# Kernel optimization log

Hardware: AMD Instinct MI355X
Metric: run time of the kernel (lower is better)

## Reference

```python
import jax, jax.numpy as jnp
import numpy as np

N_NODES = 100000
N_EDGES = 1700000  # 1.6M random edges + 100k self-loops (dgl.add_self_loop)
HID = 128
N_GRAPHS = 64
N_CLASSES = 10
T_STEPS = 5


def setup_inputs() -> dict:
    key = jax.random.key(0)
    ks = jax.random.split(key, 12)
    m = jax.random.normal(ks[0], (N_NODES,), dtype=jnp.float32)
    n_rand = N_EDGES - N_NODES
    src_r = jax.random.randint(ks[1], (n_rand,), 0, N_NODES)
    dst_r = jax.random.randint(ks[2], (n_rand,), 0, N_NODES)
    loops = jnp.arange(N_NODES)
    src = jnp.concatenate([src_r, loops])
    dst = jnp.concatenate([dst_r, loops])
    graph_ids = jnp.sort(jax.random.randint(ks[3], (N_NODES,), 0, N_GRAPHS))
    s = 0.05
    W_e = jax.random.normal(ks[4], (HID, HID), dtype=jnp.float32) * s
    b_e = jnp.zeros((HID,), dtype=jnp.float32)
    W_ih = jax.random.normal(ks[5], (3 * HID, HID), dtype=jnp.float32) * s
    b_ih = jnp.zeros((3 * HID,), dtype=jnp.float32)
    W_hh = jax.random.normal(ks[6], (3 * HID, HID), dtype=jnp.float32) * s
    b_hh = jnp.zeros((3 * HID,), dtype=jnp.float32)
    W_cls = jax.random.normal(ks[7], (N_CLASSES, HID), dtype=jnp.float32) * s
    b_cls = jnp.zeros((N_CLASSES,), dtype=jnp.float32)
    return {"m": m, "W_e": W_e, "b_e": b_e, "W_ih": W_ih, "b_ih": b_ih,
            "W_hh": W_hh, "b_hh": b_hh, "W_cls": W_cls, "b_cls": b_cls,
            "src": src, "dst": dst, "graph_ids": graph_ids, "n_graphs": N_GRAPHS}


def _gated_graph_forward(m, W_e, b_e, W_ih, b_ih, W_hh, b_hh, W_cls, b_cls,
                         src, dst, graph_ids, n_graphs):
    n_nodes = m.shape[0]
    hid = W_e.shape[0]
    # h = ndata['m'].view(-1,1), zero-padded to out_feats (DGL GatedGraphConv)
    h = jnp.zeros((n_nodes, hid), dtype=m.dtype).at[:, 0].set(m)
    for _ in range(T_STEPS):
        # single edge type: a[v] = sum_{(u,v) in E} W_e h[u] + b_e
        msg = (h @ W_e.T + b_e)[src]                       # [E, H]
        a = jax.ops.segment_sum(msg, dst, num_segments=n_nodes)
        # torch.nn.GRUCell(a, h); gate order: r, z, n
        gi = a @ W_ih.T + b_ih
        gh = h @ W_hh.T + b_hh
        i_r, i_z, i_n = jnp.split(gi, 3, axis=-1)
        h_r, h_z, h_n = jnp.split(gh, 3, axis=-1)
        r = jax.nn.sigmoid(i_r + h_r)
        z = jax.nn.sigmoid(i_z + h_z)
        n = jnp.tanh(i_n + r * h_n)
        h = (1.0 - z) * n + z * h
    h = jax.nn.relu(h)
    # dgl.mean_nodes: per-graph mean over nodes
    sums = jax.ops.segment_sum(h, graph_ids, num_segments=n_graphs)
    cnt = jax.ops.segment_sum(jnp.ones((n_nodes,), h.dtype), graph_ids,
                              num_segments=n_graphs)
    hg = sums / jnp.maximum(cnt, 1.0)[:, None]             # [G, H]
    return hg @ W_cls.T + b_cls                            # [G, C]


def reference(m, W_e, b_e, W_ih, b_ih, W_hh, b_hh, W_cls, b_cls,
              src, dst, graph_ids, n_graphs):
    return _gated_graph_forward(m, W_e, b_e, W_ih, b_ih, W_hh, b_hh,
                                W_cls, b_cls, src, dst, graph_ids, n_graphs)
```

## Files before the change

### kernel.cpp

```cpp
#include <hip/hip_runtime.h>

#define HID 128
#define G3  384
#define TSTEPS 5
#define BSHIFT 9
#define BNODES (1 << BSHIFT)
#define MAXBUK 256
#define PART_EPB 8192
#define DBUK 64

typedef unsigned int  uint;
typedef unsigned short ushort;

typedef float  f32x4  __attribute__((ext_vector_type(4)));
typedef __bf16 bf16x8 __attribute__((ext_vector_type(8)));

union B8u { uint4 u; bf16x8 b; ushort s[8]; };

static __device__ inline ushort f2bf(float f) {
  uint u = __float_as_uint(f);
  uint r = u + 0x7fffu + ((u >> 16) & 1u);
  return (ushort)(r >> 16);
}
static __device__ inline float bf2f(ushort s) {
  return __uint_as_float(((uint)s) << 16);
}

__global__ __launch_bounds__(128) void k_weights(
    const float* __restrict__ W_e, const float* __restrict__ b_e,
    const float* __restrict__ W_ih, const float* __restrict__ W_hh,
    ushort* __restrict__ Wcomb, ushort* __restrict__ Whh16, float* __restrict__ bvec,
    ushort* __restrict__ Wc0, ushort* __restrict__ Wh0)
{
  int j = blockIdx.x, t = threadIdx.x;
  if (j < G3) {
    __shared__ float row[HID];
    row[t] = W_ih[j * HID + t];
    __syncthreads();
    float acc = 0.f;
    for (int k = 0; k < HID; ++k) acc = fmaf(row[k], W_e[k * HID + t], acc);
    Wcomb[j * HID + t] = f2bf(acc);
    if (t == 0) {
      Wc0[j] = f2bf(acc);
      float b = 0.f;
      for (int k = 0; k < HID; ++k) b += row[k] * b_e[k];
      bvec[j] = b;
    }
  } else {
    int j2 = j - G3;
    Whh16[j2 * HID + t] = f2bf(W_hh[j2 * HID + t]);
    if (t == 0) Wh0[j2] = f2bf(W_hh[j2 * HID]);
  }
}

__global__ __launch_bounds__(256) void k_bh(const int* __restrict__ dst,
                                            int* __restrict__ bhist, int E) {
  __shared__ int lh[MAXBUK];
  int t = threadIdx.x;
  if (t < MAXBUK) lh[t] = 0;
  __syncthreads();
  for (int e = blockIdx.x * 256 + t; e < E; e += gridDim.x * 256)
    atomicAdd(&lh[dst[e] >> BSHIFT], 1);
  __syncthreads();
  if (t < MAXBUK && lh[t]) atomicAdd(&bhist[t], lh[t]);
}

__global__ __launch_bounds__(256) void k_bsc(const int* __restrict__ bhist,
                                             int* __restrict__ bbase,
                                             int* __restrict__ gcur,
                                             int* __restrict__ rowptr, int E, int N) {
  __shared__ int ls[MAXBUK];
  int t = threadIdx.x;
  ls[t] = bhist[t];
  __syncthreads();
  if (t == 0) {
    int run = 0;
    for (int i = 0; i < MAXBUK; ++i) {
      bbase[i] = run; gcur[i] = run; run += ls[i];
    }
    bbase[MAXBUK] = run;
    rowptr[N] = E;
  }
}

__global__ __launch_bounds__(256) void k_part(
    const int* __restrict__ src, const int* __restrict__ dst,
    int* __restrict__ gcur, uint* __restrict__ ebuf, int E) {
  __shared__ int lh[MAXBUK], lbase[MAXBUK], lcur[MAXBUK];
  int t = threadIdx.x;
  int base = blockIdx.x * PART_EPB;
  if (t < MAXBUK) lh[t] = 0;
  __syncthreads();
#pragma unroll 4
  for (int j = 0; j < PART_EPB / 256; ++j) {
    int e = base + j * 256 + t;
    if (e < E) atomicAdd(&lh[dst[e] >> BSHIFT], 1);
  }
  __syncthreads();
  if (t < MAXBUK) {
    lbase[t] = lh[t] ? atomicAdd(&gcur[t], lh[t]) : 0;
    lcur[t] = 0;
  }
  __syncthreads();
#pragma unroll 4
  for (int j = 0; j < PART_EPB / 256; ++j) {
    int e = base + j * 256 + t;
    if (e < E) {
      int d = dst[e];
      int b = d >> BSHIFT;
      int p = atomicAdd(&lcur[b], 1);
      ebuf[lbase[b] + p] = (uint)src[e] | ((uint)(d & (BNODES - 1)) << 20);
    }
  }
}

__global__ __launch_bounds__(256) void k_fill2(
    const uint* __restrict__ ebuf, const int* __restrict__ bbase,
    int* __restrict__ csrc, int* __restrict__ rowptr, int* __restrict__ deg, int N) {
  __shared__ int hcnt[BNODES];
  __shared__ int wls[4];
  int t = threadIdx.x;
  int b = blockIdx.x;
  int ebeg = bbase[b], eend = bbase[b + 1];
  for (int i = t; i < BNODES; i += 256) hcnt[i] = 0;
  __syncthreads();
  for (int e = ebeg + t; e < eend; e += 256)
    atomicAdd(&hcnt[ebuf[e] >> 20], 1);
  __syncthreads();
  const int PER = BNODES / 256;
  int lane = t & 63, wv = t >> 6;
  int x[PER]; int s = 0;
#pragma unroll
  for (int i = 0; i < PER; ++i) { x[i] = hcnt[PER * t + i]; s += x[i]; }
  int incl = s;
#pragma unroll
  for (int off = 1; off < 64; off <<= 1) {
    int u = __shfl_up(incl, off, 64);
    if (lane >= off) incl += u;
  }
  if (lane == 63) wls[wv] = incl;
  __syncthreads();
  int wbase = 0;
  for (int i = 0; i < wv; ++i) wbase += wls[i];
  int run = wbase + incl - s;
#pragma unroll
  for (int i = 0; i < PER; ++i) {
    int node = (b << BSHIFT) + PER * t + i;
    hcnt[PER * t + i] = run;
    if (node < N) { rowptr[node] = ebeg + run; deg[node] = x[i]; }
    run += x[i];
  }
  __syncthreads();
  for (int e = ebeg + t; e < eend; e += 256) {
    uint v = ebuf[e];
    int p = atomicAdd(&hcnt[v >> 20], 1);
    csrc[ebeg + p] = (int)(v & 0xFFFFFu);
  }
}

__global__ __launch_bounds__(256) void k_dhist(const int* __restrict__ deg,
                                               int* __restrict__ dhist, int N) {
  __shared__ int lh[DBUK];
  int t = threadIdx.x;
  if (t < DBUK) lh[t] = 0;
  __syncthreads();
  for (int v = blockIdx.x * 256 + t; v < N; v += gridDim.x * 256)
    atomicAdd(&lh[min(deg[v], DBUK - 1)], 1);
  __syncthreads();
  if (t < DBUK && lh[t]) atomicAdd(&dhist[t], lh[t]);
}

__global__ __launch_bounds__(64) void k_dscan(const int* __restrict__ dhist,
                                              int* __restrict__ dcur) {
  if (threadIdx.x == 0) {
    int run = 0;
    for (int i = 0; i < DBUK; ++i) { dcur[i] = run; run += dhist[i]; }
  }
}

__global__ __launch_bounds__(256) void k_dscatter(
    const int* __restrict__ deg, const int* __restrict__ rowptr,
    int* __restrict__ dcur, int* __restrict__ orig2,
    int* __restrict__ beg2, int* __restrict__ deg2s, int N) {
  __shared__ int lh[DBUK], lbase[DBUK], lcur[DBUK];
  int t = threadIdx.x;
  int v = blockIdx.x * 256 + t;
  if (t < DBUK) lh[t] = 0;
  __syncthreads();
  int d = 0, b = 0;
  bool valid = v < N;
  if (valid) {
    d = deg[v];
    b = min(d, DBUK - 1);
    atomicAdd(&lh[b], 1);
  }
  __syncthreads();
  if (t < DBUK) {
    lbase[t] = lh[t] ? atomicAdd(&dcur[t], lh[t]) : 0;
    lcur[t] = 0;
  }
  __syncthreads();
  if (valid) {
    int p = atomicAdd(&lcur[b], 1);
    int k = lbase[b] + p;
    orig2[k] = v;
    beg2[k] = rowptr[v];
    deg2s[k] = d;
  }
}

__global__ void k_minit(const float* __restrict__ m, ushort* __restrict__ m16, int N) {
  int v = blockIdx.x * 256 + threadIdx.x;
  if (v < N) m16[v] = f2bf(m[v]);
}

__global__ __launch_bounds__(256) void k_gather0(
    const int* __restrict__ rowptr, const int* __restrict__ csrc,
    const ushort* __restrict__ m16, ushort* __restrict__ hsum0, int N)
{
  int v = blockIdx.x * 256 + threadIdx.x;
  if (v >= N) return;
  int beg = rowptr[v], end = rowptr[v + 1];
  float a0 = 0.f, a1 = 0.f, a2 = 0.f, a3 = 0.f;
  int e = beg;
  for (; e + 16 <= end; e += 16) {
    a0 += (bf2f(m16[csrc[e + 0]]) + bf2f(m16[csrc[e + 4]])) +
          (bf2f(m16[csrc[e + 8]]) + bf2f(m16[csrc[e + 12]]));
    a1 += (bf2f(m16[csrc[e + 1]]) + bf2f(m16[csrc[e + 5]])) +
          (bf2f(m16[csrc[e + 9]]) + bf2f(m16[csrc[e + 13]]));
    a2 += (bf2f(m16[csrc[e + 2]]) + bf2f(m16[csrc[e + 6]])) +
          (bf2f(m16[csrc[e + 10]]) + bf2f(m16[csrc[e + 14]]));
    a3 += (bf2f(m16[csrc[e + 3]]) + bf2f(m16[csrc[e + 7]])) +
          (bf2f(m16[csrc[e + 11]]) + bf2f(m16[csrc[e + 15]]));
  }
  for (; e < end; e += 4) {
    if (e + 0 < end) a0 += bf2f(m16[csrc[e + 0]]);
    if (e + 1 < end) a1 += bf2f(m16[csrc[e + 1]]);
    if (e + 2 < end) a2 += bf2f(m16[csrc[e + 2]]);
    if (e + 3 < end) a3 += bf2f(m16[csrc[e + 3]]);
  }
  hsum0[v] = f2bf((a0 + a1) + (a2 + a3));
}

__global__ __launch_bounds__(256) void k_gru0(
    const ushort* __restrict__ hsum0, const ushort* __restrict__ m16,
    const int* __restrict__ deg,
    const ushort* __restrict__ Wc0, const ushort* __restrict__ Wh0,
    const float* __restrict__ bvec, const float* __restrict__ b_ih,
    const float* __restrict__ b_hh, ushort* __restrict__ hbn, int N)
{
  int idx = blockIdx.x * 256 + threadIdx.x;
  if (idx >= N * HID) return;
  int n = idx >> 7, d = idx & (HID - 1);
  float s0 = bf2f(hsum0[n]);
  float h0 = bf2f(m16[n]);
  float degf = (float)deg[n];
  float acc0 = s0 * bf2f(Wc0[d]);
  float acc1 = s0 * bf2f(Wc0[d + 128]);
  float acc2 = s0 * bf2f(Wc0[d + 256]);
  float acc3 = h0 * bf2f(Wh0[d]);
  float acc4 = h0 * bf2f(Wh0[d + 128]);
  float acc5 = h0 * bf2f(Wh0[d + 256]);
  float hold = (d == 0) ? h0 : 0.f;
  float ir = acc0 + degf * bvec[d] + b_ih[d];
  float iz = acc1 + degf * bvec[d + 128] + b_ih[d + 128];
  float in_ = acc2 + degf * bvec[d + 256] + b_ih[d + 256];
  float hr = acc3 + b_hh[d];
  float hz = acc4 + b_hh[d + 128];
  float hn = acc5 + b_hh[d + 256];
  float r = __builtin_amdgcn_rcpf(1.f + __expf(-(ir + hr)));
  float z = __builtin_amdgcn_rcpf(1.f + __expf(-(iz + hz)));
  float x2 = in_ + r * hn;
  float e2 = __expf(2.f * x2);
  float nv = 1.f - 2.f * __builtin_amdgcn_rcpf(e2 + 1.f);
  float hv = (1.f - z) * nv + z * hold;
  hbn[idx] = f2bf(hv);
}

static __device__ __forceinline__ void accum_range(
    const ushort* __restrict__ hb, const int* __restrict__ csrc,
    int beg, int end, int g, int i, float acc[8])
{
  int e = beg;
  for (; e + 16 <= end; e += 16) {
    int s0 = csrc[e + g];
    int s1 = csrc[e + 4 + g];
    int s2 = csrc[e + 8 + g];
    int s3 = csrc[e + 12 + g];
    B8u w0; w0.u = *(const uint4*)(hb + (size_t)s0 * HID + i * 8);
    B8u w1; w1.u = *(const uint4*)(hb + (size_t)s1 * HID + i * 8);
    B8u w2; w2.u = *(const uint4*)(hb + (size_t)s2 * HID + i * 8);
    B8u w3; w3.u = *(const uint4*)(hb + (size_t)s3 * HID + i * 8);
#pragma unroll
    for (int j = 0; j < 8; ++j)
      acc[j] += (bf2f(w0.s[j]) + bf2f(w1.s[j])) + (bf2f(w2.s[j]) + bf2f(w3.s[j]));
  }
  int rem = end - e;
  if (rem > 0) {
    int t0 = (g < rem)      ? csrc[e + g]      : -1;
    int t1 = (4 + g < rem)  ? csrc[e + 4 + g]  : -1;
    int t2 = (8 + g < rem)  ? csrc[e + 8 + g]  : -1;
    int t3 = (12 + g < rem) ? csrc[e + 12 + g] : -1;
    B8u r0, r1, r2, r3;
    if (t0 >= 0) r0.u = *(const uint4*)(hb + (size_t)t0 * HID + i * 8);
    if (t1 >= 0) r1.u = *(const uint4*)(hb + (size_t)t1 * HID + i * 8);
    if (t2 >= 0) r2.u = *(const uint4*)(hb + (size_t)t2 * HID + i * 8);
    if (t3 >= 0) r3.u = *(const uint4*)(hb + (size_t)t3 * HID + i * 8);
    if (t0 >= 0) {
#pragma unroll
      for (int j = 0; j < 8; ++j) acc[j] += bf2f(r0.s[j]);
    }
    if (t1 >= 0) {
#pragma unroll
      for (int j = 0; j < 8; ++j) acc[j] += bf2f(r1.s[j]);
    }
    if (t2 >= 0) {
#pragma unroll
      for (int j = 0; j < 8; ++j) acc[j] += bf2f(r2.s[j]);
    }
    if (t3 >= 0) {
#pragma unroll
      for (int j = 0; j < 8; ++j) acc[j] += bf2f(r3.s[j]);
    }
  }
}

static __device__ __forceinline__ void gather_strip_sorted(
    const int* __restrict__ beg2, const int* __restrict__ deg2s,
    const int* __restrict__ orig2, const int* __restrict__ csrc,
    const ushort* __restrict__ hb,
    int strip, int w, int lane, int N,
    ushort dstS[16][128], ushort dstH[16][128], int* dstDeg, int* dstOrig)
{
  int k = strip * 16 + w;
  if (k >= N) return;
  int g = lane >> 4;
  int i = lane & 15;
  int orig = orig2[k];
  int beg = beg2[k];
  int cnt = deg2s[k];
  if (g == 1)
    *(uint4*)(&dstH[w][(i ^ (w & 7)) * 8]) =
        *(const uint4*)(hb + (size_t)orig * HID + i * 8);
  if (lane == 0) dstOrig[w] = orig;
  if (lane == 32) dstDeg[w] = cnt;
  float acc[8] = {0.f, 0.f, 0.f, 0.f, 0.f, 0.f, 0.f, 0.f};
  accum_range(hb, csrc, beg, beg + cnt, g, i, acc);
#pragma unroll
  for (int j = 0; j < 8; ++j) {
    acc[j] += __shfl_xor(acc[j], 16, 64);
    acc[j] += __shfl_xor(acc[j], 32, 64);
  }
  if (g == 0) {
    uint4 ov;
    ov.x = ((uint)f2bf(acc[1]) << 16) | (uint)f2bf(acc[0]);
    ov.y = ((uint)f2bf(acc[3]) << 16) | (uint)f2bf(acc[2]);
    ov.z = ((uint)f2bf(acc[5]) << 16) | (uint)f2bf(acc[4]);
    ov.w = ((uint)f2bf(acc[7]) << 16) | (uint)f2bf(acc[6]);
    *(uint4*)(&dstS[w][(i ^ (w & 7)) * 8]) = ov;
  }
}

__global__ __launch_bounds__(1024, 4) void k_fused(
    const int* __restrict__ beg2, const int* __restrict__ deg2s,
    const int* __restrict__ orig2, const int* __restrict__ csrc,
    const ushort* __restrict__ hbc, ushort* __restrict__ hbn,
    const ushort* __restrict__ Wcomb, const ushort* __restrict__ Whh16,
    const float* __restrict__ bvec, const float* __restrict__ b_ih,
    const float* __restrict__ b_hh, int N)
{
  __shared__ float S[6][16][132];
  __shared__ ushort AT[3][2][16][128];
  __shared__ int degT[3][16];
  __shared__ int origT[3][16];
  const int tid = threadIdx.x;
  const int w = tid >> 6;
  const int lane = tid & 63;
  const int quad = lane >> 4, l16 = lane & 15;
  const int gm = w >> 3;
  const int gw = w & 7;
  const int d0 = gw * 16;

  const ushort* Wmat = gm ? Whh16 : Wcomb;
  B8u bfr[3][4];
#pragma unroll
  for (int g = 0; g < 3; ++g)
#pragma unroll
    for (int kc = 0; kc < 4; ++kc) {
      int j = (d0 + g * 128 + l16) * HID + kc * 32 + quad * 8;
      bfr[g][kc].u = *(const uint4*)(Wmat + j);
    }

  const int ecol = tid & 127, erow0 = tid >> 7;
  const float bir = b_ih[ecol], biz = b_ih[ecol + 128], bin_ = b_ih[ecol + 256];
  const float bhr = b_hh[ecol], bhz = b_hh[ecol + 128], bhn = b_hh[ecol + 256];
  const float vr = bvec[ecol], vz = bvec[ecol + 128], vn = bvec[ecol + 256];

  const int nstrip = N >> 4;
  const int G = (int)gridDim.x;
  int s = blockIdx.x;
  if (s >= nstrip) return;

  gather_strip_sorted(beg2, deg2s, orig2, csrc, hbc, s, w, lane, N,
                      AT[0][0], AT[0][1], degT[0], origT[0]);
  asm volatile("s_waitcnt lgkmcnt(0)" ::: "memory");
  __builtin_amdgcn_sched_barrier(0);
  __builtin_amdgcn_s_barrier();

  int cur = 0;
  while (true) {
    int ns = s + G;
    bool more = ns < nstrip;
    int nxt = (cur == 2) ? 0 : cur + 1;
    if (more)
      gather_strip_sorted(beg2, deg2s, orig2, csrc, hbc, ns, w, lane, N,
                          AT[nxt][0], AT[nxt][1], degT[nxt], origT[nxt]);
    B8u af[4];
#pragma unroll
    for (int kc = 0; kc < 4; ++kc)
      af[kc].u = *(const uint4*)(&AT[cur][gm][l16][(((quad + 4 * kc) ^ (l16 & 7)) * 8)]);
    f32x4 acc[3] = {};
#pragma unroll
    for (int kc = 0; kc < 4; ++kc)
#pragma unroll
      for (int g = 0; g < 3; ++g)
        acc[g] = __builtin_amdgcn_mfma_f32_16x16x32_bf16(af[kc].b, bfr[g][kc].b, acc[g], 0, 0, 0);
    __builtin_amdgcn_s_barrier();
#pragma unroll
    for (int g = 0; g < 3; ++g)
#pragma unroll
      for (int rg = 0; rg < 4; ++rg)
        S[gm * 3 + g][quad * 4 + rg][d0 + l16] = acc[g][rg];
    asm volatile("s_waitcnt lgkmcnt(0)" ::: "memory");
    __builtin_amdgcn_sched_barrier(0);
    __builtin_amdgcn_s_barrier();
    int n0 = s << 4;
#pragma unroll
    for (int k = 0; k < 2; ++k) {
      int row = erow0 + 8 * k;
      float dgf = (float)degT[cur][row];
      int og = origT[cur][row];
      int sc = (((ecol >> 3) ^ (row & 7)) * 8) + (ecol & 7);
      float hold = bf2f(AT[cur][1][row][sc]);
      float ir  = S[0][row][ecol] + dgf * vr + bir;
      float iz  = S[1][row][ecol] + dgf * vz + biz;
      float in_ = S[2][row][ecol] + dgf * vn + bin_;
      float hr  = S[3][row][ecol] + bhr;
      float hz  = S[4][row][ecol] + bhz;
      float hn  = S[5][row][ecol] + bhn;
      float r = __builtin_amdgcn_rcpf(1.f + __expf(-(ir + hr)));
      float z = __builtin_amdgcn_rcpf(1.f + __expf(-(iz + hz)));
      float x2 = in_ + r * hn;
      float e2 = __expf(2.f * x2);
      float nv = 1.f - 2.f * __builtin_amdgcn_rcpf(e2 + 1.f);
      float hv = (1.f - z) * nv + z * hold;
      if (n0 + row < N)
        hbn[(size_t)og * HID + ecol] = f2bf(hv);
    }
    if (!more) break;
    s = ns; cur = nxt;
  }
}

__global__ __launch_bounds__(64) void k_bounds(const int* __restrict__ gid,
                                               int* __restrict__ cnt, int N, int G) {
  int g = threadIdx.x;
  if (g >= G) return;
  int lo = 0, hi = N;
  while (lo < hi) { int mid = (lo + hi) >> 1; if (gid[mid] < g) lo = mid + 1; else hi = mid; }
  int lb0 = lo;
  lo = 0; hi = N;
  int g1 = g + 1;
  while (lo < hi) { int mid = (lo + hi) >> 1; if (gid[mid] < g1) lo = mid + 1; else hi = mid; }
  cnt[g] = lo - lb0;
}

#define POOL_CHUNK 96
__global__ __launch_bounds__(128) void k_pool(const ushort* __restrict__ hb,
                                              const int* __restrict__ gid,
                                              float* __restrict__ hg, int N) {
  int d = threadIdx.x;
  int start = blockIdx.x * POOL_CHUNK;
  if (start >= N) return;
  int end = min(start + POOL_CHUNK, N);
  float acc = 0.f;
  int g = gid[start];
  for (int n = start; n < end; ++n) {
    int gn = gid[n];
    if (gn != g) { unsafeAtomicAdd(&hg[g * HID + d], acc); acc = 0.f; g = gn; }
    acc += fmaxf(bf2f(hb[(size_t)n * HID + d]), 0.f);
  }
  unsafeAtomicAdd(&hg[g * HID + d], acc);
}

__global__ __launch_bounds__(640) void k_cls(const float* __restrict__ hg,
                                             const int* __restrict__ cnt,
                                             const float* __restrict__ Wc,
                                             const float* __restrict__ bc,
                                             float* __restrict__ out, int G) {
  int t = threadIdx.x;
  if (t >= G * 10) return;
  int g = t / 10, c = t % 10;
  float inv = 1.f / fmaxf((float)cnt[g], 1.f);
  float acc = 0.f;
  for (int d = 0; d < HID; ++d) acc = fmaf(hg[g * HID + d], Wc[c * HID + d], acc);
  out[t] = acc * inv + bc[c];
}

extern "C" void kernel_launch(void* const* d_in, const int* in_sizes, int n_in,
                              void* d_out, int out_size, void* d_ws, size_t ws_size,
                              hipStream_t stream) {
  const int N = in_sizes[0];
  const int E = in_sizes[9];
  const float* m    = (const float*)d_in[0];
  const float* W_e  = (const float*)d_in[1];
  const float* b_e  = (const float*)d_in[2];
  const float* W_ih = (const float*)d_in[3];
  const float* b_ih = (const float*)d_in[4];
  const float* W_hh = (const float*)d_in[5];
  const float* b_hh = (const float*)d_in[6];
  const float* W_cls = (const float*)d_in[7];
  const float* b_cls = (const float*)d_in[8];
  const int* src = (const int*)d_in[9];
  const int* dst = (const int*)d_in[10];
  const int* gid = (const int*)d_in[11];
  const int G = out_size / 10;
  float* out = (float*)d_out;

  size_t off = 0;
  auto alloc = [&](size_t b) {
    char* p = (char*)d_ws + off;
    off += (b + 255) & ~(size_t)255;
    return (void*)p;
  };
  ushort* hb0    = (ushort*)alloc((size_t)N * HID * 2);
  ushort* hb1    = (ushort*)alloc((size_t)N * HID * 2);
  int*    deg    = (int*)   alloc((size_t)N * 4);
  int*    rowptr = (int*)   alloc((size_t)(N + 1) * 4);
  int*    csrc   = (int*)   alloc((size_t)E * 4);
  uint*   ebuf   = (uint*)  alloc((size_t)E * 4);
  int*    bhist  = (int*)   alloc((size_t)MAXBUK * 4);
  int*    bbase  = (int*)   alloc((size_t)(MAXBUK + 1) * 4);
  int*    gcur   = (int*)   alloc((size_t)MAXBUK * 4);
  ushort* Wcomb  = (ushort*)alloc((size_t)G3 * HID * 2);
  ushort* Whh16  = (ushort*)alloc((size_t)G3 * HID * 2);
  float*  bvec   = (float*) alloc((size_t)G3 * 4);
  float*  hg     = (float*) alloc((size_t)G * HID * 4);
  int*    cnt    = (int*)   alloc((size_t)G * 4);
  ushort* m16    = (ushort*)alloc((size_t)N * 2);
  ushort* hsum0  = (ushort*)alloc((size_t)N * 2);
  ushort* Wc0    = (ushort*)alloc((size_t)G3 * 2);
  ushort* Wh0    = (ushort*)alloc((size_t)G3 * 2);
  int*    dhist  = (int*)   alloc((size_t)DBUK * 4);
  int*    dcur   = (int*)   alloc((size_t)DBUK * 4);
  int*    orig2  = (int*)   alloc((size_t)N * 4);
  int*    beg2   = (int*)   alloc((size_t)N * 4);
  int*    deg2s  = (int*)   alloc((size_t)N * 4);
  if (off > ws_size) return;

  const int NBUK = (N + BNODES - 1) >> BSHIFT;

  k_weights<<<2 * G3, HID, 0, stream>>>(W_e, b_e, W_ih, W_hh, Wcomb, Whh16, bvec, Wc0, Wh0);
  k_minit<<<(N + 255) / 256, 256, 0, stream>>>(m, m16, N);
  hipMemsetAsync(bhist, 0, (size_t)MAXBUK * 4, stream);
  k_bh<<<256, 256, 0, stream>>>(dst, bhist, E);
  k_bsc<<<1, MAXBUK, 0, stream>>>(bhist, bbase, gcur, rowptr, E, N);
  k_part<<<(E + PART_EPB - 1) / PART_EPB, 256, 0, stream>>>(src, dst, gcur, ebuf, E);
  k_fill2<<<NBUK, 256, 0, stream>>>(ebuf, bbase, csrc, rowptr, deg, N);

  hipMemsetAsync(dhist, 0, (size_t)DBUK * 4, stream);
  k_dhist<<<64, 256, 0, stream>>>(deg, dhist, N);
  k_dscan<<<1, 64, 0, stream>>>(dhist, dcur);
  k_dscatter<<<(N + 255) / 256, 256, 0, stream>>>(deg, rowptr, dcur, orig2, beg2, deg2s, N);

  k_gather0<<<(N + 255) / 256, 256, 0, stream>>>(rowptr, csrc, m16, hsum0, N);
  k_gru0<<<(N * HID + 255) / 256, 256, 0, stream>>>(hsum0, m16, deg, Wc0, Wh0,
                                                    bvec, b_ih, b_hh, hb1, N);

  ushort* hbc = hb1;
  ushort* hbn = hb0;
  const int nstrip = N >> 4;
  const int fuse_blocks = nstrip < 256 ? nstrip : 256;
  for (int s = 1; s < TSTEPS; ++s) {
    k_fused<<<fuse_blocks, 1024, 0, stream>>>(beg2, deg2s, orig2, csrc, hbc, hbn,
                                              Wcomb, Whh16, bvec, b_ih, b_hh, N);
    ushort* t = hbc; hbc = hbn; hbn = t;
  }

  hipMemsetAsync(hg, 0, (size_t)G * HID * 4, stream);
  k_bounds<<<1, 64, 0, stream>>>(gid, cnt, N, G);
  k_pool<<<(N + POOL_CHUNK - 1) / POOL_CHUNK, HID, 0, stream>>>(hbc, gid, hg, N);
  k_cls<<<1, 640, 0, stream>>>(hg, cnt, W_cls, b_cls, out, G);
}
```

Before: 752.9 us.

## Double-buffer GRU staging LDS and add fast path for low-degree gathers

The shared staging array S is double-buffered by loop parity, which lets the barrier before the MFMA result store be dropped so successive strips can overlap. Gathers for nodes with degree up to 31 get a specialized unrolled path that issues all neighbor index and row loads up front, raising memory-level parallelism over the generic accumulate loop. The cost is doubled LDS use for S, which may lower occupancy, plus more registers and code in the gather routine.

```diff
diff --git a/kernel.cpp b/kernel.cpp
--- a/kernel.cpp
+++ b/kernel.cpp
@@ -345,7 +345,55 @@
   if (lane == 0) dstOrig[w] = orig;
   if (lane == 32) dstDeg[w] = cnt;
   float acc[8] = {0.f, 0.f, 0.f, 0.f, 0.f, 0.f, 0.f, 0.f};
-  accum_range(hb, csrc, beg, beg + cnt, g, i, acc);
+  if (cnt <= 31) {
+    bool hm = cnt >= 16;
+    int m0 = 0, m1 = 0, m2 = 0, m3 = 0;
+    if (hm) {
+      m0 = csrc[beg + g];
+      m1 = csrc[beg + 4 + g];
+      m2 = csrc[beg + 8 + g];
+      m3 = csrc[beg + 12 + g];
+    }
+    int tb = hm ? beg + 16 : beg;
+    int rem = hm ? cnt - 16 : cnt;
+    int t0 = (g < rem)      ? csrc[tb + g]      : -1;
+    int t1 = (4 + g < rem)  ? csrc[tb + 4 + g]  : -1;
+    int t2 = (8 + g < rem)  ? csrc[tb + 8 + g]  : -1;
+    int t3 = (12 + g < rem) ? csrc[tb + 12 + g] : -1;
+    if (hm) {
+      B8u w0, w1, w2, w3;
+      w0.u = *(const uint4*)(hb + (size_t)m0 * HID + i * 8);
+      w1.u = *(const uint4*)(hb + (size_t)m1 * HID + i * 8);
+      w2.u = *(const uint4*)(hb + (size_t)m2 * HID + i * 8);
+      w3.u = *(const uint4*)(hb + (size_t)m3 * HID + i * 8);
+#pragma unroll
+      for (int j = 0; j < 8; ++j)
+        acc[j] += (bf2f(w0.s[j]) + bf2f(w1.s[j])) + (bf2f(w2.s[j]) + bf2f(w3.s[j]));
+    }
+    B8u r0, r1, r2, r3;
+    if (t0 >= 0) r0.u = *(const uint4*)(hb + (size_t)t0 * HID + i * 8);
+    if (t1 >= 0) r1.u = *(const uint4*)(hb + (size_t)t1 * HID + i * 8);
+    if (t2 >= 0) r2.u = *(const uint4*)(hb + (size_t)t2 * HID + i * 8);
+    if (t3 >= 0) r3.u = *(const uint4*)(hb + (size_t)t3 * HID + i * 8);
+    if (t0 >= 0) {
+#pragma unroll
+      for (int j = 0; j < 8; ++j) acc[j] += bf2f(r0.s[j]);
+    }
+    if (t1 >= 0) {
+#pragma unroll
+      for (int j = 0; j < 8; ++j) acc[j] += bf2f(r1.s[j]);
+    }
+    if (t2 >= 0) {
+#pragma unroll
+      for (int j = 0; j < 8; ++j) acc[j] += bf2f(r2.s[j]);
+    }
+    if (t3 >= 0) {
+#pragma unroll
+      for (int j = 0; j < 8; ++j) acc[j] += bf2f(r3.s[j]);
+    }
+  } else {
+    accum_range(hb, csrc, beg, beg + cnt, g, i, acc);
+  }
 #pragma unroll
   for (int j = 0; j < 8; ++j) {
     acc[j] += __shfl_xor(acc[j], 16, 64);
@@ -369,7 +417,7 @@
     const float* __restrict__ bvec, const float* __restrict__ b_ih,
     const float* __restrict__ b_hh, int N)
 {
-  __shared__ float S[6][16][132];
+  __shared__ float S[2][6][16][132];
   __shared__ ushort AT[3][2][16][128];
   __shared__ int degT[3][16];
   __shared__ int origT[3][16];
@@ -407,7 +455,7 @@
   __builtin_amdgcn_sched_barrier(0);
   __builtin_amdgcn_s_barrier();
 
-  int cur = 0;
+  int cur = 0, par = 0;
   while (true) {
     int ns = s + G;
     bool more = ns < nstrip;
@@ -425,12 +473,11 @@
 #pragma unroll
       for (int g = 0; g < 3; ++g)
         acc[g] = __builtin_amdgcn_mfma_f32_16x16x32_bf16(af[kc].b, bfr[g][kc].b, acc[g], 0, 0, 0);
-    __builtin_amdgcn_s_barrier();
 #pragma unroll
     for (int g = 0; g < 3; ++g)
 #pragma unroll
       for (int rg = 0; rg < 4; ++rg)
-        S[gm * 3 + g][quad * 4 + rg][d0 + l16] = acc[g][rg];
+        S[par][gm * 3 + g][quad * 4 + rg][d0 + l16] = acc[g][rg];
     asm volatile("s_waitcnt lgkmcnt(0)" ::: "memory");
     __builtin_amdgcn_sched_barrier(0);
     __builtin_amdgcn_s_barrier();
@@ -442,12 +489,12 @@
       int og = origT[cur][row];
       int sc = (((ecol >> 3) ^ (row & 7)) * 8) + (ecol & 7);
       float hold = bf2f(AT[cur][1][row][sc]);
-      float ir  = S[0][row][ecol] + dgf * vr + bir;
-      float iz  = S[1][row][ecol] + dgf * vz + biz;
-      float in_ = S[2][row][ecol] + dgf * vn + bin_;
-      float hr  = S[3][row][ecol] + bhr;
-      float hz  = S[4][row][ecol] + bhz;
-      float hn  = S[5][row][ecol] + bhn;
+      float ir  = S[par][0][row][ecol] + dgf * vr + bir;
+      float iz  = S[par][1][row][ecol] + dgf * vz + biz;
+      float in_ = S[par][2][row][ecol] + dgf * vn + bin_;
+      float hr  = S[par][3][row][ecol] + bhr;
+      float hz  = S[par][4][row][ecol] + bhz;
+      float hn  = S[par][5][row][ecol] + bhn;
       float r = __builtin_amdgcn_rcpf(1.f + __expf(-(ir + hr)));
       float z = __builtin_amdgcn_rcpf(1.f + __expf(-(iz + hz)));
       float x2 = in_ + r * hn;
@@ -458,7 +505,7 @@
         hbn[(size_t)og * HID + ecol] = f2bf(hv);
     }
     if (!more) break;
-    s = ns; cur = nxt;
+    s = ns; cur = nxt; par ^= 1;
   }
 }
 
```

After: 778.6 us. 1.03x slower.

## Issue neighbor-row gathers as async global-to-LDS loads overlapped with MFMA

Applied to the files above, without the earlier changes.

Replaces the call to the next-strip gather with an inline version that issues up to 20 neighbor-row loads per wave directly into a new LDS staging buffer via global_load_lds. These loads are in flight while the current strip's MFMAs and the S stores run. The remaining few neighbors are loaded into registers, and high-degree nodes fall back to the existing accumulate routine. This aims to hide gather latency behind compute, at the cost of about 80KB of extra LDS, which may reduce occupancy under the 1024-thread launch bound.

```diff
diff --git a/kernel.cpp b/kernel.cpp
--- a/kernel.cpp
+++ b/kernel.cpp
@@ -24,6 +24,12 @@
 }
 static __device__ inline float bf2f(ushort s) {
   return __uint_as_float(((uint)s) << 16);
+}
+
+static __device__ __forceinline__ void gload_lds16(const void* g, void* l) {
+  __builtin_amdgcn_global_load_lds(
+      (const __attribute__((address_space(1))) uint*)g,
+      (__attribute__((address_space(3))) uint*)l, 16, 0, 0);
 }
 
 __global__ __launch_bounds__(128) void k_weights(
@@ -373,6 +379,7 @@
   __shared__ ushort AT[3][2][16][128];
   __shared__ int degT[3][16];
   __shared__ int origT[3][16];
+  __shared__ ushort STG[16][5][512];
   const int tid = threadIdx.x;
   const int w = tid >> 6;
   const int lane = tid & 63;
@@ -412,25 +419,105 @@
     int ns = s + G;
     bool more = ns < nstrip;
     int nxt = (cur == 2) ? 0 : cur + 1;
-    if (more)
-      gather_strip_sorted(beg2, deg2s, orig2, csrc, hbc, ns, w, lane, N,
-                          AT[nxt][0], AT[nxt][1], degT[nxt], origT[nxt]);
+    int cntP = 0, begP = 0, i5 = -1, i6 = -1, i7 = -1;
+    uint4 hrow = make_uint4(0, 0, 0, 0);
+    if (more) {
+      int k2 = ns * 16 + w;
+      int orig = orig2[k2];
+      begP = beg2[k2];
+      cntP = deg2s[k2];
+      if (lane == 0) origT[nxt][w] = orig;
+      if (lane == 32) degT[nxt][w] = cntP;
+      if (quad == 1) hrow = *(const uint4*)(hbc + (size_t)orig * HID + l16 * 8);
+      if (cntP <= 31) {
+#pragma unroll
+        for (int j = 0; j < 5; ++j)
+          if (4 * j + quad < cntP) {
+            int ix = csrc[begP + 4 * j + quad];
+            gload_lds16(hbc + (size_t)ix * HID + l16 * 8, &STG[w][j][0]);
+          }
+        i5 = (20 + quad < cntP) ? csrc[begP + 20 + quad] : -1;
+        i6 = (24 + quad < cntP) ? csrc[begP + 24 + quad] : -1;
+        i7 = (28 + quad < cntP) ? csrc[begP + 28 + quad] : -1;
+      }
+    }
     B8u af[4];
 #pragma unroll
     for (int kc = 0; kc < 4; ++kc)
       af[kc].u = *(const uint4*)(&AT[cur][gm][l16][(((quad + 4 * kc) ^ (l16 & 7)) * 8)]);
-    f32x4 acc[3] = {};
+    f32x4 acc3[3] = {};
 #pragma unroll
     for (int kc = 0; kc < 4; ++kc)
 #pragma unroll
       for (int g = 0; g < 3; ++g)
-        acc[g] = __builtin_amdgcn_mfma_f32_16x16x32_bf16(af[kc].b, bfr[g][kc].b, acc[g], 0, 0, 0);
+        acc3[g] = __builtin_amdgcn_mfma_f32_16x16x32_bf16(af[kc].b, bfr[g][kc].b, acc3[g], 0, 0, 0);
     __builtin_amdgcn_s_barrier();
 #pragma unroll
     for (int g = 0; g < 3; ++g)
 #pragma unroll
       for (int rg = 0; rg < 4; ++rg)
-        S[gm * 3 + g][quad * 4 + rg][d0 + l16] = acc[g][rg];
+        S[gm * 3 + g][quad * 4 + rg][d0 + l16] = acc3[g][rg];
+    if (more) {
+      float acc[8] = {0.f, 0.f, 0.f, 0.f, 0.f, 0.f, 0.f, 0.f};
+      if (cntP <= 31) {
+        asm volatile("s_waitcnt vmcnt(0)" ::: "memory");
+        __builtin_amdgcn_sched_barrier(0);
+        if (cntP >= 16) {
+          B8u c0, c1, c2, c3;
+          c0.u = *(const uint4*)&STG[w][0][lane * 8];
+          c1.u = *(const uint4*)&STG[w][1][lane * 8];
+          c2.u = *(const uint4*)&STG[w][2][lane * 8];
+          c3.u = *(const uint4*)&STG[w][3][lane * 8];
+#pragma unroll
+          for (int j = 0; j < 8; ++j)
+            acc[j] += (bf2f(c0.s[j]) + bf2f(c1.s[j])) + (bf2f(c2.s[j]) + bf2f(c3.s[j]));
+        } else {
+#pragma unroll
+          for (int jj = 0; jj < 4; ++jj)
+            if (4 * jj + quad < cntP) {
+              B8u cv; cv.u = *(const uint4*)&STG[w][jj][lane * 8];
+#pragma unroll
+              for (int j = 0; j < 8; ++j) acc[j] += bf2f(cv.s[j]);
+            }
+        }
+        if (16 + quad < cntP) {
+          B8u c4; c4.u = *(const uint4*)&STG[w][4][lane * 8];
+#pragma unroll
+          for (int j = 0; j < 8; ++j) acc[j] += bf2f(c4.s[j]);
+        }
+        if (i5 >= 0) {
+          B8u rv; rv.u = *(const uint4*)(hbc + (size_t)i5 * HID + l16 * 8);
+#pragma unroll
+          for (int j = 0; j < 8; ++j) acc[j] += bf2f(rv.s[j]);
+        }
+        if (i6 >= 0) {
+          B8u rv; rv.u = *(const uint4*)(hbc + (size_t)i6 * HID + l16 * 8);
+#pragma unroll
+          for (int j = 0; j < 8; ++j) acc[j] += bf2f(rv.s[j]);
+        }
+        if (i7 >= 0) {
+          B8u rv; rv.u = *(const uint4*)(hbc + (size_t)i7 * HID + l16 * 8);
+#pragma unroll
+          for (int j = 0; j < 8; ++j) acc[j] += bf2f(rv.s[j]);
+        }
+      } else {
+        accum_range(hbc, csrc, begP, begP + cntP, quad, l16, acc);
+      }
+#pragma unroll
+      for (int j = 0; j < 8; ++j) {
+        acc[j] += __shfl_xor(acc[j], 16, 64);
+        acc[j] += __shfl_xor(acc[j], 32, 64);
+      }
+      if (quad == 0) {
+        uint4 ov;
+        ov.x = ((uint)f2bf(acc[1]) << 16) | (uint)f2bf(acc[0]);
+        ov.y = ((uint)f2bf(acc[3]) << 16) | (uint)f2bf(acc[2]);
+        ov.z = ((uint)f2bf(acc[5]) << 16) | (uint)f2bf(acc[4]);
+        ov.w = ((uint)f2bf(acc[7]) << 16) | (uint)f2bf(acc[6]);
+        *(uint4*)(&AT[nxt][0][w][(l16 ^ (w & 7)) * 8]) = ov;
+      }
+      if (quad == 1) *(uint4*)(&AT[nxt][1][w][(l16 ^ (w & 7)) * 8]) = hrow;
+    }
     asm volatile("s_waitcnt lgkmcnt(0)" ::: "memory");
     __builtin_amdgcn_sched_barrier(0);
     __builtin_amdgcn_s_barrier();
```

Measured after the change: 825.6 us. 9.7% more time.
